# Kernel tuning notes

Measured on AMD Instinct MI355X. Metric: run time of the kernel, lower is better.

Reference implementation:

```python
import jax, jax.numpy as jnp
import numpy as np

B, T, H = 256, 2048, 128


def setup_inputs() -> dict:
    key = jax.random.key(0)
    k1, k2 = jax.random.split(key)
    x = jax.random.normal(k1, (B, T), dtype=jnp.float32)
    # Dense weight for concat([h, x_t]) of width H+1 -> H; scaled ~1/sqrt(fan_in)
    W = jax.random.normal(k2, (H + 1, H), dtype=jnp.float32) * (1.0 / np.sqrt(H + 1))
    b = jnp.zeros((H,), dtype=jnp.float32)
    return {"x": x, "W": W, "b": b}


def reference(x, W, b):
    # x: [B, T] scalar-feature sequence; W: [H+1, H]; b: [H]
    Bn, Tn = x.shape
    Hn = b.shape[0]

    def step(carry, x_t):
        h, c = carry  # each [B, H]
        # so all four gate splits are the identical tensor g.
        g = jnp.concatenate([h, x_t[:, None]], axis=-1) @ W + b  # [B, H]
        sg = jax.nn.sigmoid(g)
        c_new = sg * c + sg * g          # sigmoid(forget)*c + sigmoid(input)*cell_bar
        h_new = sg * c_new               # sigmoid(output)*c_new (no tanh, updated c)
        return (h_new, c_new), h_new

    h0 = jnp.zeros((Bn, Hn), dtype=x.dtype)
    c0 = jnp.zeros((Bn, Hn), dtype=x.dtype)
    _, hs = jax.lax.scan(step, (h0, c0), jnp.swapaxes(x, 0, 1))  # hs: [T, B, H]
    return jnp.transpose(hs, (1, 0, 2))  # [B, T, H]
```

## Files before the change

kernel.cpp:

```cpp
#include <hip/hip_runtime.h>


#define BB 256
#define TT 2048
#define HH 128
#define NT 512

#define LOADW(k) \
    float4 w##k = make_float4(W[(kbase + 4*(k)+0)*HH + jc], W[(kbase + 4*(k)+1)*HH + jc], \
                              W[(kbase + 4*(k)+2)*HH + jc], W[(kbase + 4*(k)+3)*HH + jc]);

#define KEEPW(k) \
    asm volatile("" : "+v"(w##k.x), "+v"(w##k.y), "+v"(w##k.z), "+v"(w##k.w));

#define MAC4(k) { \
    const float4 hv = hrd[(k)]; \
    a0 = fmaf(hv.x, w##k.x, a0); \
    a1 = fmaf(hv.y, w##k.y, a1); \
    a2 = fmaf(hv.z, w##k.z, a2); \
    a3 = fmaf(hv.w, w##k.w, a3); }

__device__ __forceinline__ float quad_bfly_sum(float v) {
    int o1 = __builtin_amdgcn_mov_dpp(__float_as_int(v), 0xB1, 0xf, 0xf, true);
    float p = v + __int_as_float(o1);
    int o2 = __builtin_amdgcn_mov_dpp(__float_as_int(p), 0x4E, 0xf, 0xf, true);
    return p + __int_as_float(o2);
}

__global__ __launch_bounds__(NT)
__attribute__((amdgpu_waves_per_eu(2, 2)))
void lstm_scan_kernel(
    const float* __restrict__ x,
    const float* __restrict__ W,
    const float* __restrict__ b,
    float* __restrict__ out)
{
    const int tid   = threadIdx.x;
    const int lane  = tid & 63;
    const int wave  = tid >> 6;
    const int s     = lane & 3;
    const int jc    = (wave << 4) | (lane >> 2);
    const int kbase = s << 5;
    const int batch = blockIdx.x;

    __shared__ float xs[TT];
    __shared__ float hrep[2][4][132];

    for (int t = tid; t < TT; t += NT) {
        xs[t] = x[(size_t)batch * TT + t];
    }
    for (int i = tid; i < 4 * 132; i += NT) {
        (&hrep[0][0][0])[i] = 0.0f;
    }

    LOADW(0) LOADW(1) LOADW(2) LOADW(3) LOADW(4) LOADW(5) LOADW(6) LOADW(7)
    KEEPW(0) KEEPW(1) KEEPW(2) KEEPW(3) KEEPW(4) KEEPW(5) KEEPW(6) KEEPW(7)

    const float wx   = (s == 0) ? W[HH * HH + jc] : 0.0f;
    const float bias = (s == 0) ? b[jc]           : 0.0f;

    float c = 0.0f;
    float* outp = out + (size_t)batch * TT * HH + jc;

    const float4* hrd0 = (const float4*)&hrep[0][s][kbase];
    const float4* hrd1 = (const float4*)&hrep[1][s][kbase];
    float* hw0 = &hrep[0][s][jc];
    float* hw1 = &hrep[1][s][jc];

    __syncthreads();

    for (int t = 0; t < TT; ++t) {
        const float4* hrd = (t & 1) ? hrd1 : hrd0;

        float a0 = fmaf(xs[t], wx, bias);
        float a1 = 0.0f, a2 = 0.0f, a3 = 0.0f;
        MAC4(0) MAC4(1) MAC4(2) MAC4(3) MAC4(4) MAC4(5) MAC4(6) MAC4(7)

        const float g = quad_bfly_sum((a0 + a1) + (a2 + a3));

        const float sg = 1.0f / (1.0f + __expf(-g));
        c = sg * (c + g);
        const float hn = sg * c;

        *((t & 1) ? hw0 : hw1) = hn;
        if (s == 0) outp[(size_t)t * HH] = hn;

        asm volatile("s_waitcnt lgkmcnt(0)" ::: "memory");
        __builtin_amdgcn_s_barrier();
        asm volatile("" ::: "memory");
    }
}

extern "C" void kernel_launch(void* const* d_in, const int* in_sizes, int n_in,
                              void* d_out, int out_size, void* d_ws, size_t ws_size,
                              hipStream_t stream) {
    const float* x = (const float*)d_in[0];
    const float* W = (const float*)d_in[1];
    const float* b = (const float*)d_in[2];
    float* out = (float*)d_out;

    lstm_scan_kernel<<<BB, NT, 0, stream>>>(x, W, b, out);
}
```

Measured before the change: 980.7 us.

## Repartition matvec across 16 k-slices per row with DPP row reductions

```diff
diff --git a/kernel.cpp b/kernel.cpp
--- a/kernel.cpp
+++ b/kernel.cpp
@@ -7,25 +7,22 @@
 #define NT 512
 
 #define LOADW(k) \
-    float4 w##k = make_float4(W[(kbase + 4*(k)+0)*HH + jc], W[(kbase + 4*(k)+1)*HH + jc], \
-                              W[(kbase + 4*(k)+2)*HH + jc], W[(kbase + 4*(k)+3)*HH + jc]);
+    float4 w##k = *(const float4*)&W[(kb + (k)) * HH + c0];
 
 #define KEEPW(k) \
     asm volatile("" : "+v"(w##k.x), "+v"(w##k.y), "+v"(w##k.z), "+v"(w##k.w));
 
-#define MAC4(k) { \
-    const float4 hv = hrd[(k)]; \
-    a0 = fmaf(hv.x, w##k.x, a0); \
-    a1 = fmaf(hv.y, w##k.y, a1); \
-    a2 = fmaf(hv.z, w##k.z, a2); \
-    a3 = fmaf(hv.w, w##k.w, a3); }
+#define MACR(k, hv) { \
+    a0 = fmaf((hv), w##k.x, a0); \
+    a1 = fmaf((hv), w##k.y, a1); \
+    a2 = fmaf((hv), w##k.z, a2); \
+    a3 = fmaf((hv), w##k.w, a3); }
 
-__device__ __forceinline__ float quad_bfly_sum(float v) {
-    int o1 = __builtin_amdgcn_mov_dpp(__float_as_int(v), 0xB1, 0xf, 0xf, true);
-    float p = v + __int_as_float(o1);
-    int o2 = __builtin_amdgcn_mov_dpp(__float_as_int(p), 0x4E, 0xf, 0xf, true);
-    return p + __int_as_float(o2);
-}
+#define RORADD(v, ctrl) { \
+    int _o = __builtin_amdgcn_mov_dpp(__float_as_int(v), (ctrl), 0xf, 0xf, true); \
+    (v) += __int_as_float(_o); }
+
+#define ROWSUM(v) RORADD(v, 0x128) RORADD(v, 0x124) RORADD(v, 0x122) RORADD(v, 0x121)
 
 __global__ __launch_bounds__(NT)
 __attribute__((amdgpu_waves_per_eu(2, 2)))
@@ -38,52 +35,65 @@
     const int tid   = threadIdx.x;
     const int lane  = tid & 63;
     const int wave  = tid >> 6;
-    const int s     = lane & 3;
-    const int jc    = (wave << 4) | (lane >> 2);
-    const int kbase = s << 5;
+    const int s     = lane & 15;
+    const int m     = lane >> 4;
+    const int q     = s & 3;
+    const int c0    = (wave << 4) | (m << 2);
+    const int csel  = c0 + q;
+    const int kb    = s << 3;
     const int batch = blockIdx.x;
 
     __shared__ float xs[TT];
-    __shared__ float hrep[2][4][132];
+    __shared__ float hb[2][16 * 12];
 
     for (int t = tid; t < TT; t += NT) {
         xs[t] = x[(size_t)batch * TT + t];
     }
-    for (int i = tid; i < 4 * 132; i += NT) {
-        (&hrep[0][0][0])[i] = 0.0f;
-    }
+    if (tid < 2 * 16 * 12) ((float*)hb)[tid] = 0.0f;
 
     LOADW(0) LOADW(1) LOADW(2) LOADW(3) LOADW(4) LOADW(5) LOADW(6) LOADW(7)
     KEEPW(0) KEEPW(1) KEEPW(2) KEEPW(3) KEEPW(4) KEEPW(5) KEEPW(6) KEEPW(7)
 
-    const float wx   = (s == 0) ? W[HH * HH + jc] : 0.0f;
-    const float bias = (s == 0) ? b[jc]           : 0.0f;
+    const float wxv = W[HH * HH + csel];
+    const float bv  = b[csel];
 
     float c = 0.0f;
-    float* outp = out + (size_t)batch * TT * HH + jc;
+    const bool writer = (s < 4);
+    float* outp = out + (size_t)batch * TT * HH + csel;
 
-    const float4* hrd0 = (const float4*)&hrep[0][s][kbase];
-    const float4* hrd1 = (const float4*)&hrep[1][s][kbase];
-    float* hw0 = &hrep[0][s][jc];
-    float* hw1 = &hrep[1][s][jc];
+    const float4* hr0 = (const float4*)&hb[0][12 * s];
+    const float4* hr1 = (const float4*)&hb[1][12 * s];
+    const int hwidx = 12 * (csel >> 3) + (csel & 7);
+    float* hw0 = &hb[0][hwidx];
+    float* hw1 = &hb[1][hwidx];
 
     __syncthreads();
 
     for (int t = 0; t < TT; ++t) {
-        const float4* hrd = (t & 1) ? hrd1 : hrd0;
+        const float4* hr = (t & 1) ? hr1 : hr0;
+        const float4 hA = hr[0];
+        const float4 hB = hr[1];
+        const float xt = xs[t];
 
-        float a0 = fmaf(xs[t], wx, bias);
-        float a1 = 0.0f, a2 = 0.0f, a3 = 0.0f;
-        MAC4(0) MAC4(1) MAC4(2) MAC4(3) MAC4(4) MAC4(5) MAC4(6) MAC4(7)
+        float a0 = 0.0f, a1 = 0.0f, a2 = 0.0f, a3 = 0.0f;
+        MACR(0, hA.x) MACR(1, hA.y) MACR(2, hA.z) MACR(3, hA.w)
+        MACR(4, hB.x) MACR(5, hB.y) MACR(6, hB.z) MACR(7, hB.w)
 
-        const float g = quad_bfly_sum((a0 + a1) + (a2 + a3));
+        ROWSUM(a0) ROWSUM(a1) ROWSUM(a2) ROWSUM(a3)
+
+        const float tA   = (q & 1) ? a1 : a0;
+        const float tB   = (q & 1) ? a3 : a2;
+        const float gsum = (q & 2) ? tB : tA;
+        const float g    = fmaf(xt, wxv, gsum + bv);
 
         const float sg = 1.0f / (1.0f + __expf(-g));
         c = sg * (c + g);
         const float hn = sg * c;
 
-        *((t & 1) ? hw0 : hw1) = hn;
-        if (s == 0) outp[(size_t)t * HH] = hn;
+        if (writer) {
+            *((t & 1) ? hw0 : hw1) = hn;
+            outp[(size_t)t * HH] = hn;
+        }
 
         asm volatile("s_waitcnt lgkmcnt(0)" ::: "memory");
         __builtin_amdgcn_s_barrier();
```

Result: faster. 865.3 us (-11.8%).
